# Performance work log

Measured on AMD Instinct MI355X. Metric: run time of the kernel, lower is better.

Reference implementation:

```python
import jax, jax.numpy as jnp
import numpy as np

H = 256  # hidden/feature size (input_size == output_size)
B = 512  # batch
T = 256  # sequence length


def _lstm_cell(x_t, h, c, W_ih, W_hh, b_ih, b_hh):
    # PyTorch gate order: input, forget, cell(g), output
    z = x_t @ W_ih.T + h @ W_hh.T + (b_ih + b_hh)
    i, f, g, o = jnp.split(z, 4, axis=-1)
    c_new = jax.nn.sigmoid(f) * c + jax.nn.sigmoid(i) * jnp.tanh(g)
    h_new = jax.nn.sigmoid(o) * jnp.tanh(c_new)
    return h_new, c_new


def setup_inputs() -> dict:
    key = jax.random.key(0)
    ks = jax.random.split(key, 11)
    s = 1.0 / np.sqrt(H)
    u = lambda k, shape: jax.random.uniform(k, shape, jnp.float32, -s, s)
    return {
        "x": jax.random.normal(ks[0], (B, T, H), jnp.float32),
        "W_ih1": u(ks[1], (4 * H, H)),
        "W_hh1": u(ks[2], (4 * H, H)),
        "b_ih1": u(ks[3], (4 * H,)),
        "b_hh1": u(ks[4], (4 * H,)),
        "W1": u(ks[5], (H, H)),
        "b1": u(ks[6], (H,)),
        "W_ih2": u(ks[7], (4 * H, H)),
        "W_hh2": u(ks[8], (4 * H, H)),
        "b_ih2": u(ks[9], (4 * H,)),
        "b_hh2": u(ks[10], (4 * H,)),
    }


def reference(x, W_ih1, W_hh1, b_ih1, b_hh1, W1, b1, W_ih2, W_hh2, b_ih2, b_hh2):
    Bx, Tx, Hx = x.shape
    xs = jnp.swapaxes(x, 0, 1)  # (T, B, H)

    # Encoder LSTM: only final (h, c) is used downstream
    def enc_step(carry, x_t):
        h, c = carry
        h, c = _lstm_cell(x_t, h, c, W_ih1, W_hh1, b_ih1, b_hh1)
        return (h, c), None

    zeros = jnp.zeros((Bx, Hx), x.dtype)
    (h1, c1), _ = jax.lax.scan(enc_step, (zeros, zeros), xs)

    # x_end = Linear(h1)
    x_end = h1 @ W1.T + b1  # (B, H)

    # Decoder LSTM: feeds its own output back, T steps
    def dec_step(carry, _):
        out, h, c = carry
        h, c = _lstm_cell(out, h, c, W_ih2, W_hh2, b_ih2, b_hh2)
        return (h, h, c), h

    _, outs = jax.lax.scan(dec_step, (x_end, h1, c1), None, length=Tx)  # (T, B, H)

    # Faithful index replay: x_out[:, T-2-i] = outs[i]; i = T-1 hits index -1,
    # overwriting the x_end initially written at position T-1.
    # => x_out[:, j] = outs[T-2-j] for j < T-1, x_out[:, T-1] = outs[T-1]
    x_out_t = jnp.concatenate([outs[: Tx - 1][::-1], outs[Tx - 1 :]], axis=0)  # (T, B, H)
    return jnp.swapaxes(x_out_t, 0, 1)  # (B, T, H)
```

## Files before the change

### kernel.cpp

```cpp
#include <hip/hip_runtime.h>
#include <stdint.h>


#define H_ 256
#define B_ 512
#define T_ 256

typedef short short8 __attribute__((ext_vector_type(8)));
typedef float f32x4 __attribute__((ext_vector_type(4)));

__device__ __forceinline__ short f2bf(float f) {
  union { float f; uint32_t u; } v; v.f = f;
  uint32_t r = (v.u + 0x7FFFu + ((v.u >> 16) & 1u)) >> 16;
  return (short)(uint16_t)r;
}

__device__ __forceinline__ short8 load8f_bf(const float* __restrict__ p) {
  const float4 a = *(const float4*)p;
  const float4 b = *(const float4*)(p + 4);
  short8 r;
  r[0]=f2bf(a.x); r[1]=f2bf(a.y); r[2]=f2bf(a.z); r[3]=f2bf(a.w);
  r[4]=f2bf(b.x); r[5]=f2bf(b.y); r[6]=f2bf(b.z); r[7]=f2bf(b.w);
  return r;
}

__device__ __forceinline__ short8 load8f_bf_sum(const float* __restrict__ p,
                                                const float* __restrict__ q) {
  const float4 a = *(const float4*)p, b = *(const float4*)(p + 4);
  const float4 c = *(const float4*)q, d = *(const float4*)(q + 4);
  short8 r;
  r[0]=f2bf(a.x+c.x); r[1]=f2bf(a.y+c.y); r[2]=f2bf(a.z+c.z); r[3]=f2bf(a.w+c.w);
  r[4]=f2bf(b.x+d.x); r[5]=f2bf(b.y+d.y); r[6]=f2bf(b.z+d.z); r[7]=f2bf(b.w+d.w);
  return r;
}

__device__ __forceinline__ short8 coh_load16(const uint16_t* p) {
  union { uint64_t u[2]; short8 v; } r;
  const uint64_t* q = (const uint64_t*)p;
  r.u[0] = __hip_atomic_load(q,     __ATOMIC_RELAXED, __HIP_MEMORY_SCOPE_AGENT);
  r.u[1] = __hip_atomic_load(q + 1, __ATOMIC_RELAXED, __HIP_MEMORY_SCOPE_AGENT);
  return r.v;
}

__device__ __forceinline__ float sigm(float x)  { return 1.0f / (1.0f + __expf(-x)); }
__device__ __forceinline__ float tanh_(float x) { return 1.0f - 2.0f / (1.0f + __expf(2.0f * x)); }

__global__ __launch_bounds__(256, 1) void encdec_kernel(
    const float* __restrict__ x,
    const float* __restrict__ Wih1, const float* __restrict__ Whh1,
    const float* __restrict__ bih1, const float* __restrict__ bhh1,
    const float* __restrict__ W1,   const float* __restrict__ b1,
    const float* __restrict__ Wih2, const float* __restrict__ Whh2,
    const float* __restrict__ bih2, const float* __restrict__ bhh2,
    float* __restrict__ out,
    uint32_t* __restrict__ bar,
    uint16_t* __restrict__ hbuf)
{
  __shared__ uint16_t hsh[32][16];
  __shared__ float    osh[32][16];

  const int tid = threadIdx.x;
  const int l   = tid & 63;
  const int w   = tid >> 6;
  const int blk = blockIdx.x;
  const int gid = (blk & 7) | ((blk >> 7) << 3);
  const int mid = (blk >> 3) & 15;
  const int bg  = gid * 32;
  const int c0  = mid * 16 + w * 4;

  const int nl   = l & 15;
  const int kc   = l >> 4;
  const int gate = nl >> 2;
  const int cm   = nl & 3;
  const int colg = c0 + cm;
  const int grow = gate * H_ + colg;

  uint32_t* flags = bar + (size_t)gid * 512;
  const int myflag = (mid * 4 + w) * 8;

  uint16_t* slot0 = hbuf;
  uint16_t* slot1 = hbuf + (size_t)B_ * H_;
  uint16_t* slot2 = hbuf + (size_t)2 * B_ * H_;

  auto arrive = [&](int target) {
    asm volatile("s_waitcnt vmcnt(0)" ::: "memory");
    if (l == 0)
      __hip_atomic_store(&flags[myflag], (uint32_t)target,
                         __ATOMIC_RELAXED, __HIP_MEMORY_SCOPE_AGENT);
  };
  auto poll = [&](int target) {
    int g = 0;
    while ((int)__hip_atomic_load(&flags[l * 8], __ATOMIC_RELAXED,
                                  __HIP_MEMORY_SCOPE_AGENT) < target) {
      __builtin_amdgcn_s_sleep(1);
      if (++g > 2000000) break;
    }
    asm volatile("" ::: "memory");
  };
  auto ldsbar = [&]() {
    asm volatile("s_waitcnt lgkmcnt(0)\n\ts_barrier" ::: "memory");
  };

  short8 fwa[8], fwb[8];
#pragma unroll
  for (int kt = 0; kt < 8; ++kt) {
    fwa[kt] = load8f_bf(Wih1 + (size_t)grow * H_ + kt * 32 + kc * 8);
    fwb[kt] = load8f_bf(Whh1 + (size_t)grow * H_ + kt * 32 + kc * 8);
  }
  float bias = bih1[grow] + bhh1[grow];

  float cst[2][4];
#pragma unroll
  for (int mt = 0; mt < 2; ++mt)
#pragma unroll
    for (int r = 0; r < 4; ++r) cst[mt][r] = 0.0f;

  auto epi = [&](const f32x4* acc, float bias_, bool wout) {
    const int rb = (l & 48) | cm;
#pragma unroll
    for (int mt = 0; mt < 2; ++mt) {
      float hn = 0.f;
#pragma unroll
      for (int r = 0; r < 4; ++r) {
        float z = acc[mt][r] + bias_;
        float a = (gate == 2) ? tanh_(z) : sigm(z);
        float ti = __shfl(a, rb,      64);
        float tf = __shfl(a, rb | 4,  64);
        float tg = __shfl(a, rb | 8,  64);
        float to = __shfl(a, rb | 12, 64);
        float cn = tf * cst[mt][r] + ti * tg;
        cst[mt][r] = cn;
        if (r == gate) hn = to * tanh_(cn);
      }
      hsh[mt * 16 + kc * 4 + gate][w * 4 + cm] = (uint16_t)f2bf(hn);
      if (wout) osh[mt * 16 + kc * 4 + gate][w * 4 + cm] = hn;
    }
  };

  const int gb = tid >> 3;
  const int gc = tid & 7;

  f32x4 accN[2];
  auto xmfma = [&](int t) {
#pragma unroll
    for (int mt = 0; mt < 2; ++mt) {
      f32x4 a = {0.f, 0.f, 0.f, 0.f};
      const float* xr = x + ((size_t)(bg + mt * 16 + nl) * T_ + t) * H_ + kc * 8;
#pragma unroll
      for (int kt = 0; kt < 8; ++kt) {
        short8 af = load8f_bf(xr + kt * 32);
        a = __builtin_amdgcn_mfma_f32_16x16x32_bf16(af, fwa[kt], a, 0, 0, 0);
      }
      accN[mt] = a;
    }
  };
  xmfma(0);

  for (int t = 0; t < T_; ++t) {
    f32x4 acc[2] = { accN[0], accN[1] };
    if (t > 0) {
      poll(t);
      const uint16_t* hs = (t & 1) ? slot1 : slot0;
      short8 hA[2][8];
#pragma unroll
      for (int mt = 0; mt < 2; ++mt)
#pragma unroll
        for (int kt = 0; kt < 8; ++kt)
          hA[mt][kt] = coh_load16(hs + (size_t)(bg + mt * 16 + nl) * H_ + kt * 32 + kc * 8);
#pragma unroll
      for (int mt = 0; mt < 2; ++mt)
#pragma unroll
        for (int kt = 0; kt < 8; ++kt)
          acc[mt] = __builtin_amdgcn_mfma_f32_16x16x32_bf16(hA[mt][kt], fwb[kt], acc[mt], 0, 0, 0);
    }
    epi(acc, bias, false);
    ldsbar();
    uint16_t* hw = ((t + 1) & 1) ? slot1 : slot0;
    {
      uint32_t hv = *(const uint32_t*)&hsh[gb][gc * 2];
      __hip_atomic_store((uint32_t*)&hw[(size_t)(bg + gb) * H_ + mid * 16 + gc * 2], hv,
                         __ATOMIC_RELAXED, __HIP_MEMORY_SCOPE_AGENT);
    }
    arrive(t + 1);
    if (t + 1 < T_) xmfma(t + 1);
  }

  poll(T_);
  {
    const int xcol = mid * 16 + nl;
    short8 fw1[8];
#pragma unroll
    for (int kt = 0; kt < 8; ++kt)
      fw1[kt] = load8f_bf(W1 + (size_t)xcol * H_ + kt * 32 + kc * 8);
    f32x4 acc[2] = { {0.f,0.f,0.f,0.f}, {0.f,0.f,0.f,0.f} };
#pragma unroll
    for (int mt = 0; mt < 2; ++mt) {
      const uint16_t* hr = slot0 + (size_t)(bg + mt * 16 + nl) * H_ + kc * 8;
#pragma unroll
      for (int kt = 0; kt < 8; ++kt) {
        short8 af = coh_load16(hr + kt * 32);
        acc[mt] = __builtin_amdgcn_mfma_f32_16x16x32_bf16(af, fw1[kt], acc[mt], 0, 0, 0);
      }
    }
    float bb = b1[xcol];
    if (w == 0) {
#pragma unroll
      for (int mt = 0; mt < 2; ++mt)
#pragma unroll
        for (int r = 0; r < 4; ++r) {
          int b = bg + mt * 16 + kc * 4 + r;
          __hip_atomic_store(&slot2[(size_t)b * H_ + mid * 16 + nl], (uint16_t)f2bf(acc[mt][r] + bb),
                             __ATOMIC_RELAXED, __HIP_MEMORY_SCOPE_AGENT);
        }
    }
  }
  arrive(T_ + 1);

  short8 fwa2[8], fwb2[8], fws[8];
#pragma unroll
  for (int kt = 0; kt < 8; ++kt) {
    const float* pa = Wih2 + (size_t)grow * H_ + kt * 32 + kc * 8;
    const float* pb = Whh2 + (size_t)grow * H_ + kt * 32 + kc * 8;
    fwa2[kt] = load8f_bf(pa);
    fwb2[kt] = load8f_bf(pb);
    fws[kt]  = load8f_bf_sum(pa, pb);
  }
  bias = bih2[grow] + bhh2[grow];
  poll(T_ + 1);

  {
    f32x4 acc[2] = { {0.f,0.f,0.f,0.f}, {0.f,0.f,0.f,0.f} };
    short8 hA[2][8], hB[2][8];
#pragma unroll
    for (int mt = 0; mt < 2; ++mt)
#pragma unroll
      for (int kt = 0; kt < 8; ++kt) {
        const size_t ro = (size_t)(bg + mt * 16 + nl) * H_ + kt * 32 + kc * 8;
        hA[mt][kt] = coh_load16(slot2 + ro);
        hB[mt][kt] = coh_load16(slot0 + ro);
      }
#pragma unroll
    for (int mt = 0; mt < 2; ++mt)
#pragma unroll
      for (int kt = 0; kt < 8; ++kt) {
        acc[mt] = __builtin_amdgcn_mfma_f32_16x16x32_bf16(hA[mt][kt], fwa2[kt], acc[mt], 0, 0, 0);
        acc[mt] = __builtin_amdgcn_mfma_f32_16x16x32_bf16(hB[mt][kt], fwb2[kt], acc[mt], 0, 0, 0);
      }
    epi(acc, bias, true);
    ldsbar();
    uint32_t hv = *(const uint32_t*)&hsh[gb][gc * 2];
    uint64_t ov = *(const uint64_t*)&osh[gb][gc * 2];
    __hip_atomic_store((uint32_t*)&slot1[(size_t)(bg + gb) * H_ + mid * 16 + gc * 2], hv,
                       __ATOMIC_RELAXED, __HIP_MEMORY_SCOPE_AGENT);
    arrive(T_ + 2);
    *(uint64_t*)&out[((size_t)(bg + gb) * T_ + (T_ - 2)) * H_ + mid * 16 + gc * 2] = ov;
  }

  for (int t = 1; t < T_; ++t) {
    poll(T_ + 1 + t);
    const uint16_t* hs = (t & 1) ? slot1 : slot0;
    f32x4 acc[2] = { {0.f,0.f,0.f,0.f}, {0.f,0.f,0.f,0.f} };
    short8 hA[2][8];
#pragma unroll
    for (int mt = 0; mt < 2; ++mt)
#pragma unroll
      for (int kt = 0; kt < 8; ++kt)
        hA[mt][kt] = coh_load16(hs + (size_t)(bg + mt * 16 + nl) * H_ + kt * 32 + kc * 8);
#pragma unroll
    for (int mt = 0; mt < 2; ++mt)
#pragma unroll
      for (int kt = 0; kt < 8; ++kt)
        acc[mt] = __builtin_amdgcn_mfma_f32_16x16x32_bf16(hA[mt][kt], fws[kt], acc[mt], 0, 0, 0);

    epi(acc, bias, true);
    ldsbar();
    const int j = (t == T_ - 1) ? (T_ - 1) : (T_ - 2 - t);
    uint32_t hv = *(const uint32_t*)&hsh[gb][gc * 2];
    uint64_t ov = *(const uint64_t*)&osh[gb][gc * 2];
    if (t + 1 < T_) {
      uint16_t* hw = ((t + 1) & 1) ? slot1 : slot0;
      __hip_atomic_store((uint32_t*)&hw[(size_t)(bg + gb) * H_ + mid * 16 + gc * 2], hv,
                         __ATOMIC_RELAXED, __HIP_MEMORY_SCOPE_AGENT);
      arrive(T_ + 2 + t);
    }
    *(uint64_t*)&out[((size_t)(bg + gb) * T_ + j) * H_ + mid * 16 + gc * 2] = ov;
  }
}

extern "C" void kernel_launch(void* const* d_in, const int* in_sizes, int n_in,
                              void* d_out, int out_size, void* d_ws, size_t ws_size,
                              hipStream_t stream) {
  const float* x    = (const float*)d_in[0];
  const float* Wih1 = (const float*)d_in[1];
  const float* Whh1 = (const float*)d_in[2];
  const float* bih1 = (const float*)d_in[3];
  const float* bhh1 = (const float*)d_in[4];
  const float* W1   = (const float*)d_in[5];
  const float* b1   = (const float*)d_in[6];
  const float* Wih2 = (const float*)d_in[7];
  const float* Whh2 = (const float*)d_in[8];
  const float* bih2 = (const float*)d_in[9];
  const float* bhh2 = (const float*)d_in[10];
  float* out = (float*)d_out;

  uint32_t* bar  = (uint32_t*)d_ws;
  uint16_t* hbuf = (uint16_t*)((char*)d_ws + 32768);

  hipLaunchKernelGGL(encdec_kernel, dim3(256), dim3(256), 0, stream,
                     x, Wih1, Whh1, bih1, bhh1, W1, b1, Wih2, Whh2, bih2, bhh2,
                     out, bar, hbuf);
}
```

Baseline: 4.418 ms.

## Add XCD-local fast coherence path and stage recurrent h through swizzled LDS

At startup, blocks in a batch group check whether they all run on the same XCD and test a handshake. If they pass, the kernel uses sc0-only loads and stores in inline asm for flags and h exchange in place of agent-scope atomics, on the idea that L2 coherence within one XCD is enough. Each step now loads h into a swizzled LDS tile with wide dwordx4 loads, shared across the waves, so each wave no longer issues many small 64-bit atomic loads. The cost is an extra LDS barrier per step, an untested fast path whose correctness depends on how blocks are placed, and a shorter poll timeout.

```diff
diff --git a/kernel.cpp b/kernel.cpp
--- a/kernel.cpp
+++ b/kernel.cpp
@@ -8,6 +8,7 @@
 
 typedef short short8 __attribute__((ext_vector_type(8)));
 typedef float f32x4 __attribute__((ext_vector_type(4)));
+typedef uint32_t u32x4 __attribute__((ext_vector_type(4)));
 
 __device__ __forceinline__ short f2bf(float f) {
   union { float f; uint32_t u; } v; v.f = f;
@@ -34,18 +35,46 @@
   return r;
 }
 
-__device__ __forceinline__ short8 coh_load16(const uint16_t* p) {
-  union { uint64_t u[2]; short8 v; } r;
-  const uint64_t* q = (const uint64_t*)p;
-  r.u[0] = __hip_atomic_load(q,     __ATOMIC_RELAXED, __HIP_MEMORY_SCOPE_AGENT);
-  r.u[1] = __hip_atomic_load(q + 1, __ATOMIC_RELAXED, __HIP_MEMORY_SCOPE_AGENT);
-  return r.v;
+__device__ __forceinline__ void fence4u(u32x4 (&a)[4]) {
+  asm volatile("s_waitcnt vmcnt(0)"
+               : "+v"(a[0]), "+v"(a[1]), "+v"(a[2]), "+v"(a[3]));
+}
+
+template<bool FAST>
+__device__ __forceinline__ uint32_t ldflag(const uint32_t* p) {
+  if constexpr (FAST) {
+    uint32_t r;
+    asm volatile("global_load_dword %0, %1, off sc0\n\ts_waitcnt vmcnt(0)"
+                 : "=v"(r) : "v"((uint64_t)p));
+    return r;
+  } else {
+    return __hip_atomic_load(p, __ATOMIC_RELAXED, __HIP_MEMORY_SCOPE_AGENT);
+  }
+}
+
+template<bool FAST>
+__device__ __forceinline__ void st4(uint32_t* p, uint32_t v) {
+  if constexpr (FAST)
+    asm volatile("global_store_dword %0, %1, off sc0"
+                 :: "v"((uint64_t)p), "v"(v) : "memory");
+  else
+    __hip_atomic_store(p, v, __ATOMIC_RELAXED, __HIP_MEMORY_SCOPE_AGENT);
+}
+
+template<bool FAST>
+__device__ __forceinline__ void st2(uint16_t* p, uint16_t v) {
+  if constexpr (FAST)
+    asm volatile("global_store_short %0, %1, off sc0"
+                 :: "v"((uint64_t)p), "v"((uint32_t)v) : "memory");
+  else
+    __hip_atomic_store(p, v, __ATOMIC_RELAXED, __HIP_MEMORY_SCOPE_AGENT);
 }
 
 __device__ __forceinline__ float sigm(float x)  { return 1.0f / (1.0f + __expf(-x)); }
 __device__ __forceinline__ float tanh_(float x) { return 1.0f - 2.0f / (1.0f + __expf(2.0f * x)); }
 
-__global__ __launch_bounds__(256, 1) void encdec_kernel(
+template<bool FAST>
+__device__ __forceinline__ void body(
     const float* __restrict__ x,
     const float* __restrict__ Wih1, const float* __restrict__ Whh1,
     const float* __restrict__ bih1, const float* __restrict__ bhh1,
@@ -54,11 +83,10 @@
     const float* __restrict__ bih2, const float* __restrict__ bhh2,
     float* __restrict__ out,
     uint32_t* __restrict__ bar,
-    uint16_t* __restrict__ hbuf)
+    uint16_t* __restrict__ hbuf,
+    uint16_t (&hsh)[32][16], float (&osh)[32][16],
+    uint16_t (&hstage)[32][256], uint16_t (&hstage2)[32][256])
 {
-  __shared__ uint16_t hsh[32][16];
-  __shared__ float    osh[32][16];
-
   const int tid = threadIdx.x;
   const int l   = tid & 63;
   const int w   = tid >> 6;
@@ -75,6 +103,8 @@
   const int colg = c0 + cm;
   const int grow = gate * H_ + colg;
 
+  const int POLL_MAX = FAST ? 50000 : 2000000;
+
   uint32_t* flags = bar + (size_t)gid * 512;
   const int myflag = (mid * 4 + w) * 8;
 
@@ -84,21 +114,49 @@
 
   auto arrive = [&](int target) {
     asm volatile("s_waitcnt vmcnt(0)" ::: "memory");
-    if (l == 0)
-      __hip_atomic_store(&flags[myflag], (uint32_t)target,
-                         __ATOMIC_RELAXED, __HIP_MEMORY_SCOPE_AGENT);
+    if (l == 0) st4<FAST>(&flags[myflag], (uint32_t)target);
   };
   auto poll = [&](int target) {
     int g = 0;
-    while ((int)__hip_atomic_load(&flags[l * 8], __ATOMIC_RELAXED,
-                                  __HIP_MEMORY_SCOPE_AGENT) < target) {
+    while ((int)ldflag<FAST>(&flags[l * 8]) < target) {
       __builtin_amdgcn_s_sleep(1);
-      if (++g > 2000000) break;
+      if (++g > POLL_MAX) break;
     }
     asm volatile("" ::: "memory");
   };
   auto ldsbar = [&]() {
     asm volatile("s_waitcnt lgkmcnt(0)\n\ts_barrier" ::: "memory");
+  };
+
+  auto stage_to = [&](uint16_t (&dst)[32][256], const uint16_t* hs) {
+    const int rb_ = tid >> 3;
+    const int cb_ = (tid & 7) * 4;
+    const uint16_t* src = hs + (size_t)(bg + rb_) * H_ + cb_ * 8;
+    if constexpr (FAST) {
+      u32x4 v[4];
+#pragma unroll
+      for (int i = 0; i < 4; ++i)
+        asm volatile("global_load_dwordx4 %0, %1, off sc0"
+                     : "=v"(v[i]) : "v"((uint64_t)(src + i * 8)));
+      fence4u(v);
+#pragma unroll
+      for (int i = 0; i < 4; ++i)
+        *(u32x4*)&dst[rb_][(((cb_ + i) ^ (rb_ & 7)) * 8)] = v[i];
+    } else {
+#pragma unroll
+      for (int i = 0; i < 4; ++i) {
+        union { uint64_t u[2]; u32x4 v; } r;
+        const uint64_t* q = (const uint64_t*)(src + i * 8);
+        r.u[0] = __hip_atomic_load(q,     __ATOMIC_RELAXED, __HIP_MEMORY_SCOPE_AGENT);
+        r.u[1] = __hip_atomic_load(q + 1, __ATOMIC_RELAXED, __HIP_MEMORY_SCOPE_AGENT);
+        *(u32x4*)&dst[rb_][(((cb_ + i) ^ (rb_ & 7)) * 8)] = r.v;
+      }
+    }
+  };
+  auto frag = [&](uint16_t (&src)[32][256], int mt, int kt) -> short8 {
+    const int row = mt * 16 + nl;
+    const int ch  = (kt * 4 + kc) ^ (row & 7);
+    return *(const short8*)&src[row][ch * 8];
   };
 
   short8 fwa[8], fwb[8];
@@ -161,31 +219,28 @@
     if (t > 0) {
       poll(t);
       const uint16_t* hs = (t & 1) ? slot1 : slot0;
-      short8 hA[2][8];
+      stage_to(hstage, hs);
+      ldsbar();
 #pragma unroll
       for (int mt = 0; mt < 2; ++mt)
 #pragma unroll
         for (int kt = 0; kt < 8; ++kt)
-          hA[mt][kt] = coh_load16(hs + (size_t)(bg + mt * 16 + nl) * H_ + kt * 32 + kc * 8);
-#pragma unroll
-      for (int mt = 0; mt < 2; ++mt)
-#pragma unroll
-        for (int kt = 0; kt < 8; ++kt)
-          acc[mt] = __builtin_amdgcn_mfma_f32_16x16x32_bf16(hA[mt][kt], fwb[kt], acc[mt], 0, 0, 0);
+          acc[mt] = __builtin_amdgcn_mfma_f32_16x16x32_bf16(frag(hstage, mt, kt), fwb[kt], acc[mt], 0, 0, 0);
     }
     epi(acc, bias, false);
     ldsbar();
     uint16_t* hw = ((t + 1) & 1) ? slot1 : slot0;
     {
       uint32_t hv = *(const uint32_t*)&hsh[gb][gc * 2];
-      __hip_atomic_store((uint32_t*)&hw[(size_t)(bg + gb) * H_ + mid * 16 + gc * 2], hv,
-                         __ATOMIC_RELAXED, __HIP_MEMORY_SCOPE_AGENT);
+      st4<FAST>((uint32_t*)&hw[(size_t)(bg + gb) * H_ + mid * 16 + gc * 2], hv);
     }
     arrive(t + 1);
     if (t + 1 < T_) xmfma(t + 1);
   }
 
   poll(T_);
+  stage_to(hstage, slot0);
+  ldsbar();
   {
     const int xcol = mid * 16 + nl;
     short8 fw1[8];
@@ -194,14 +249,10 @@
       fw1[kt] = load8f_bf(W1 + (size_t)xcol * H_ + kt * 32 + kc * 8);
     f32x4 acc[2] = { {0.f,0.f,0.f,0.f}, {0.f,0.f,0.f,0.f} };
 #pragma unroll
-    for (int mt = 0; mt < 2; ++mt) {
-      const uint16_t* hr = slot0 + (size_t)(bg + mt * 16 + nl) * H_ + kc * 8;
-#pragma unroll
-      for (int kt = 0; kt < 8; ++kt) {
-        short8 af = coh_load16(hr + kt * 32);
-        acc[mt] = __builtin_amdgcn_mfma_f32_16x16x32_bf16(af, fw1[kt], acc[mt], 0, 0, 0);
-      }
-    }
+    for (int mt = 0; mt < 2; ++mt)
+#pragma unroll
+      for (int kt = 0; kt < 8; ++kt)
+        acc[mt] = __builtin_amdgcn_mfma_f32_16x16x32_bf16(frag(hstage, mt, kt), fw1[kt], acc[mt], 0, 0, 0);
     float bb = b1[xcol];
     if (w == 0) {
 #pragma unroll
@@ -209,8 +260,7 @@
 #pragma unroll
         for (int r = 0; r < 4; ++r) {
           int b = bg + mt * 16 + kc * 4 + r;
-          __hip_atomic_store(&slot2[(size_t)b * H_ + mid * 16 + nl], (uint16_t)f2bf(acc[mt][r] + bb),
-                             __ATOMIC_RELAXED, __HIP_MEMORY_SCOPE_AGENT);
+          st2<FAST>(&slot2[(size_t)b * H_ + mid * 16 + nl], (uint16_t)f2bf(acc[mt][r] + bb));
         }
     }
   }
@@ -229,29 +279,21 @@
   poll(T_ + 1);
 
   {
+    stage_to(hstage2, slot2);
+    ldsbar();
     f32x4 acc[2] = { {0.f,0.f,0.f,0.f}, {0.f,0.f,0.f,0.f} };
-    short8 hA[2][8], hB[2][8];
 #pragma unroll
     for (int mt = 0; mt < 2; ++mt)
 #pragma unroll
       for (int kt = 0; kt < 8; ++kt) {
-        const size_t ro = (size_t)(bg + mt * 16 + nl) * H_ + kt * 32 + kc * 8;
-        hA[mt][kt] = coh_load16(slot2 + ro);
-        hB[mt][kt] = coh_load16(slot0 + ro);
-      }
-#pragma unroll
-    for (int mt = 0; mt < 2; ++mt)
-#pragma unroll
-      for (int kt = 0; kt < 8; ++kt) {
-        acc[mt] = __builtin_amdgcn_mfma_f32_16x16x32_bf16(hA[mt][kt], fwa2[kt], acc[mt], 0, 0, 0);
-        acc[mt] = __builtin_amdgcn_mfma_f32_16x16x32_bf16(hB[mt][kt], fwb2[kt], acc[mt], 0, 0, 0);
+        acc[mt] = __builtin_amdgcn_mfma_f32_16x16x32_bf16(frag(hstage2, mt, kt), fwa2[kt], acc[mt], 0, 0, 0);
+        acc[mt] = __builtin_amdgcn_mfma_f32_16x16x32_bf16(frag(hstage,  mt, kt), fwb2[kt], acc[mt], 0, 0, 0);
       }
     epi(acc, bias, true);
     ldsbar();
     uint32_t hv = *(const uint32_t*)&hsh[gb][gc * 2];
     uint64_t ov = *(const uint64_t*)&osh[gb][gc * 2];
-    __hip_atomic_store((uint32_t*)&slot1[(size_t)(bg + gb) * H_ + mid * 16 + gc * 2], hv,
-                       __ATOMIC_RELAXED, __HIP_MEMORY_SCOPE_AGENT);
+    st4<FAST>((uint32_t*)&slot1[(size_t)(bg + gb) * H_ + mid * 16 + gc * 2], hv);
     arrive(T_ + 2);
     *(uint64_t*)&out[((size_t)(bg + gb) * T_ + (T_ - 2)) * H_ + mid * 16 + gc * 2] = ov;
   }
@@ -259,18 +301,14 @@
   for (int t = 1; t < T_; ++t) {
     poll(T_ + 1 + t);
     const uint16_t* hs = (t & 1) ? slot1 : slot0;
+    stage_to(hstage, hs);
+    ldsbar();
     f32x4 acc[2] = { {0.f,0.f,0.f,0.f}, {0.f,0.f,0.f,0.f} };
-    short8 hA[2][8];
 #pragma unroll
     for (int mt = 0; mt < 2; ++mt)
 #pragma unroll
       for (int kt = 0; kt < 8; ++kt)
-        hA[mt][kt] = coh_load16(hs + (size_t)(bg + mt * 16 + nl) * H_ + kt * 32 + kc * 8);
-#pragma unroll
-    for (int mt = 0; mt < 2; ++mt)
-#pragma unroll
-      for (int kt = 0; kt < 8; ++kt)
-        acc[mt] = __builtin_amdgcn_mfma_f32_16x16x32_bf16(hA[mt][kt], fws[kt], acc[mt], 0, 0, 0);
+        acc[mt] = __builtin_amdgcn_mfma_f32_16x16x32_bf16(frag(hstage, mt, kt), fws[kt], acc[mt], 0, 0, 0);
 
     epi(acc, bias, true);
     ldsbar();
@@ -279,12 +317,83 @@
     uint64_t ov = *(const uint64_t*)&osh[gb][gc * 2];
     if (t + 1 < T_) {
       uint16_t* hw = ((t + 1) & 1) ? slot1 : slot0;
-      __hip_atomic_store((uint32_t*)&hw[(size_t)(bg + gb) * H_ + mid * 16 + gc * 2], hv,
-                         __ATOMIC_RELAXED, __HIP_MEMORY_SCOPE_AGENT);
+      st4<FAST>((uint32_t*)&hw[(size_t)(bg + gb) * H_ + mid * 16 + gc * 2], hv);
       arrive(T_ + 2 + t);
     }
     *(uint64_t*)&out[((size_t)(bg + gb) * T_ + j) * H_ + mid * 16 + gc * 2] = ov;
   }
+}
+
+__global__ __launch_bounds__(256, 1) void encdec_kernel(
+    const float* __restrict__ x,
+    const float* __restrict__ Wih1, const float* __restrict__ Whh1,
+    const float* __restrict__ bih1, const float* __restrict__ bhh1,
+    const float* __restrict__ W1,   const float* __restrict__ b1,
+    const float* __restrict__ Wih2, const float* __restrict__ Whh2,
+    const float* __restrict__ bih2, const float* __restrict__ bhh2,
+    float* __restrict__ out,
+    uint32_t* __restrict__ bar,
+    uint16_t* __restrict__ hbuf)
+{
+  __shared__ __align__(16) uint16_t hstage [32][256];
+  __shared__ __align__(16) uint16_t hstage2[32][256];
+  __shared__ uint16_t hsh[32][16];
+  __shared__ float    osh[32][16];
+
+  const int tid = threadIdx.x;
+  const int l   = tid & 63;
+  const int blk = blockIdx.x;
+  const int gid = (blk & 7) | ((blk >> 7) << 3);
+  const int mid = (blk >> 3) & 15;
+
+  uint32_t* xw = bar + (size_t)gid * 512;
+
+  const uint32_t my_xcc = (uint32_t)__builtin_amdgcn_s_getreg(6164) & 0xffu;
+  if (tid == 0)
+    __hip_atomic_store(&xw[mid * 8 + 1], 0x100u | my_xcc,
+                       __ATOMIC_RELAXED, __HIP_MEMORY_SCOPE_AGENT);
+  uint32_t pv = 0; int g = 0; bool seen = true;
+  for (;;) {
+    pv = __hip_atomic_load(&xw[(l & 15) * 8 + 1],
+                           __ATOMIC_RELAXED, __HIP_MEMORY_SCOPE_AGENT);
+    if (pv & 0x100u) break;
+    __builtin_amdgcn_s_sleep(1);
+    if (++g > 1000000) { seen = false; break; }
+  }
+  const bool same_xcd = __all((int)(seen && ((pv & 0xffu) == my_xcc)));
+
+  int verdict = 0;
+  if (same_xcd) {
+    if (tid == 0) st4<true>(&xw[mid * 8 + 2], 0xA5A5u);
+    g = 0; bool s2 = true;
+    for (;;) {
+      uint32_t qv = ldflag<true>(&xw[(l & 15) * 8 + 2]);
+      if (qv == 0xA5A5u) break;
+      __builtin_amdgcn_s_sleep(1);
+      if (++g > 20000) { s2 = false; break; }
+    }
+    verdict = __all((int)s2) ? 1 : 0;
+  }
+
+  if (tid == 0)
+    __hip_atomic_store(&xw[mid * 8 + 3], 0x200u | (uint32_t)verdict,
+                       __ATOMIC_RELAXED, __HIP_MEMORY_SCOPE_AGENT);
+  uint32_t vv = 0; g = 0; seen = true;
+  for (;;) {
+    vv = __hip_atomic_load(&xw[(l & 15) * 8 + 3],
+                           __ATOMIC_RELAXED, __HIP_MEMORY_SCOPE_AGENT);
+    if (vv & 0x200u) break;
+    __builtin_amdgcn_s_sleep(1);
+    if (++g > 1000000) { seen = false; break; }
+  }
+  const bool fast = __all((int)(seen && (vv & 1u)));
+
+  if (fast)
+    body<true>(x, Wih1, Whh1, bih1, bhh1, W1, b1, Wih2, Whh2, bih2, bhh2,
+               out, bar, hbuf, hsh, osh, hstage, hstage2);
+  else
+    body<false>(x, Wih1, Whh1, bih1, bhh1, W1, b1, Wih2, Whh2, bih2, bhh2,
+                out, bar, hbuf, hsh, osh, hstage, hstage2);
 }
 
 extern "C" void kernel_launch(void* const* d_in, const int* in_sizes, int n_in,
```

Measured after the change: 6.398 ms. +44.8%, slower.

## Replace flag barrier with tagged-data polling on hidden-state exchange buffers

Applied to the files above, without the earlier changes.

Removes the separate arrive/poll flag handshake between blocks and instead packs a step tag into the upper 32 bits of each 64-bit store of hidden-state data. Consumers spin-load the whole hidden tile and retry until every tag matches the expected step, so data and readiness arrive in one memory round trip instead of a flag wait followed by a data load. The cost is that the exchange buffers double in size, each retry reloads the full tile, and the s_waitcnt before the flag write is gone. The x_end handoff also reuses slot1 with a tag, and the decoder's first step reuses the h1 tile already held in registers.

```diff
diff --git a/kernel.cpp b/kernel.cpp
--- a/kernel.cpp
+++ b/kernel.cpp
@@ -34,14 +34,6 @@
   return r;
 }
 
-__device__ __forceinline__ short8 coh_load16(const uint16_t* p) {
-  union { uint64_t u[2]; short8 v; } r;
-  const uint64_t* q = (const uint64_t*)p;
-  r.u[0] = __hip_atomic_load(q,     __ATOMIC_RELAXED, __HIP_MEMORY_SCOPE_AGENT);
-  r.u[1] = __hip_atomic_load(q + 1, __ATOMIC_RELAXED, __HIP_MEMORY_SCOPE_AGENT);
-  return r.v;
-}
-
 __device__ __forceinline__ float sigm(float x)  { return 1.0f / (1.0f + __expf(-x)); }
 __device__ __forceinline__ float tanh_(float x) { return 1.0f - 2.0f / (1.0f + __expf(2.0f * x)); }
 
@@ -53,8 +45,7 @@
     const float* __restrict__ Wih2, const float* __restrict__ Whh2,
     const float* __restrict__ bih2, const float* __restrict__ bhh2,
     float* __restrict__ out,
-    uint32_t* __restrict__ bar,
-    uint16_t* __restrict__ hbuf)
+    uint64_t* __restrict__ s0, uint64_t* __restrict__ s1)
 {
   __shared__ uint16_t hsh[32][16];
   __shared__ float    osh[32][16];
@@ -66,36 +57,59 @@
   const int gid = (blk & 7) | ((blk >> 7) << 3);
   const int mid = (blk >> 3) & 15;
   const int bg  = gid * 32;
-  const int c0  = mid * 16 + w * 4;
 
   const int nl   = l & 15;
   const int kc   = l >> 4;
   const int gate = nl >> 2;
   const int cm   = nl & 3;
-  const int colg = c0 + cm;
+  const int colg = mid * 16 + w * 4 + cm;
   const int grow = gate * H_ + colg;
 
-  uint32_t* flags = bar + (size_t)gid * 512;
-  const int myflag = (mid * 4 + w) * 8;
-
-  uint16_t* slot0 = hbuf;
-  uint16_t* slot1 = hbuf + (size_t)B_ * H_;
-  uint16_t* slot2 = hbuf + (size_t)2 * B_ * H_;
-
-  auto arrive = [&](int target) {
-    asm volatile("s_waitcnt vmcnt(0)" ::: "memory");
-    if (l == 0)
-      __hip_atomic_store(&flags[myflag], (uint32_t)target,
-                         __ATOMIC_RELAXED, __HIP_MEMORY_SCOPE_AGENT);
-  };
-  auto poll = [&](int target) {
-    int g = 0;
-    while ((int)__hip_atomic_load(&flags[l * 8], __ATOMIC_RELAXED,
-                                  __HIP_MEMORY_SCOPE_AGENT) < target) {
-      __builtin_amdgcn_s_sleep(1);
-      if (++g > 2000000) break;
-    }
-    asm volatile("" ::: "memory");
+  uint64_t* slot[2] = { s0, s1 };
+  int budget = 1 << 20;
+
+  auto ld_tile = [&](const uint64_t* s, uint32_t tag, short8 (&hA)[2][8]) {
+    uint64_t raw[2][8][4];
+    for (;;) {
+#pragma unroll
+      for (int mt = 0; mt < 2; ++mt) {
+        const uint64_t* rp = s + (size_t)(bg + mt * 16 + nl) * (H_ / 2) + kc * 4;
+#pragma unroll
+        for (int kt = 0; kt < 8; ++kt)
+#pragma unroll
+          for (int i = 0; i < 4; ++i)
+            raw[mt][kt][i] = __hip_atomic_load(rp + kt * 16 + i,
+                                               __ATOMIC_RELAXED, __HIP_MEMORY_SCOPE_AGENT);
+      }
+      uint32_t bad = 0;
+#pragma unroll
+      for (int mt = 0; mt < 2; ++mt)
+#pragma unroll
+        for (int kt = 0; kt < 8; ++kt)
+#pragma unroll
+          for (int i = 0; i < 4; ++i)
+            bad |= ((uint32_t)(raw[mt][kt][i] >> 32)) ^ tag;
+      if (__all(bad == 0) || --budget < 0) break;
+    }
+#pragma unroll
+    for (int mt = 0; mt < 2; ++mt)
+#pragma unroll
+      for (int kt = 0; kt < 8; ++kt) {
+        union { uint32_t d[4]; short8 v; } u;
+#pragma unroll
+        for (int i = 0; i < 4; ++i) u.d[i] = (uint32_t)raw[mt][kt][i];
+        hA[mt][kt] = u.v;
+      }
+  };
+
+  const int gb = tid >> 3;
+  const int gc = tid & 7;
+
+  auto stg = [&](uint64_t* s, uint32_t tag) {
+    uint32_t pay = (uint32_t)hsh[gb][gc * 2] | ((uint32_t)hsh[gb][gc * 2 + 1] << 16);
+    __hip_atomic_store(s + (size_t)(bg + gb) * (H_ / 2) + mid * 8 + gc,
+                       ((uint64_t)tag << 32) | pay,
+                       __ATOMIC_RELAXED, __HIP_MEMORY_SCOPE_AGENT);
   };
   auto ldsbar = [&]() {
     asm volatile("s_waitcnt lgkmcnt(0)\n\ts_barrier" ::: "memory");
@@ -137,9 +151,6 @@
     }
   };
 
-  const int gb = tid >> 3;
-  const int gc = tid & 7;
-
   f32x4 accN[2];
   auto xmfma = [&](int t) {
 #pragma unroll
@@ -159,14 +170,8 @@
   for (int t = 0; t < T_; ++t) {
     f32x4 acc[2] = { accN[0], accN[1] };
     if (t > 0) {
-      poll(t);
-      const uint16_t* hs = (t & 1) ? slot1 : slot0;
       short8 hA[2][8];
-#pragma unroll
-      for (int mt = 0; mt < 2; ++mt)
-#pragma unroll
-        for (int kt = 0; kt < 8; ++kt)
-          hA[mt][kt] = coh_load16(hs + (size_t)(bg + mt * 16 + nl) * H_ + kt * 32 + kc * 8);
+      ld_tile(slot[t & 1], (uint32_t)t, hA);
 #pragma unroll
       for (int mt = 0; mt < 2; ++mt)
 #pragma unroll
@@ -175,17 +180,12 @@
     }
     epi(acc, bias, false);
     ldsbar();
-    uint16_t* hw = ((t + 1) & 1) ? slot1 : slot0;
-    {
-      uint32_t hv = *(const uint32_t*)&hsh[gb][gc * 2];
-      __hip_atomic_store((uint32_t*)&hw[(size_t)(bg + gb) * H_ + mid * 16 + gc * 2], hv,
-                         __ATOMIC_RELAXED, __HIP_MEMORY_SCOPE_AGENT);
-    }
-    arrive(t + 1);
+    stg(slot[(t + 1) & 1], (uint32_t)(t + 1));
     if (t + 1 < T_) xmfma(t + 1);
   }
 
-  poll(T_);
+  short8 h1f[2][8];
+  ld_tile(slot[0], 256u, h1f);
   {
     const int xcol = mid * 16 + nl;
     short8 fw1[8];
@@ -194,27 +194,29 @@
       fw1[kt] = load8f_bf(W1 + (size_t)xcol * H_ + kt * 32 + kc * 8);
     f32x4 acc[2] = { {0.f,0.f,0.f,0.f}, {0.f,0.f,0.f,0.f} };
 #pragma unroll
-    for (int mt = 0; mt < 2; ++mt) {
-      const uint16_t* hr = slot0 + (size_t)(bg + mt * 16 + nl) * H_ + kc * 8;
-#pragma unroll
-      for (int kt = 0; kt < 8; ++kt) {
-        short8 af = coh_load16(hr + kt * 32);
-        acc[mt] = __builtin_amdgcn_mfma_f32_16x16x32_bf16(af, fw1[kt], acc[mt], 0, 0, 0);
-      }
-    }
+    for (int mt = 0; mt < 2; ++mt)
+#pragma unroll
+      for (int kt = 0; kt < 8; ++kt)
+        acc[mt] = __builtin_amdgcn_mfma_f32_16x16x32_bf16(h1f[mt][kt], fw1[kt], acc[mt], 0, 0, 0);
     float bb = b1[xcol];
     if (w == 0) {
 #pragma unroll
       for (int mt = 0; mt < 2; ++mt)
 #pragma unroll
         for (int r = 0; r < 4; ++r) {
-          int b = bg + mt * 16 + kc * 4 + r;
-          __hip_atomic_store(&slot2[(size_t)b * H_ + mid * 16 + nl], (uint16_t)f2bf(acc[mt][r] + bb),
-                             __ATOMIC_RELAXED, __HIP_MEMORY_SCOPE_AGENT);
+          float me = acc[mt][r] + bb;
+          float nb = __shfl(me, l ^ 1, 64);
+          if (!(nl & 1)) {
+            uint32_t pay = (uint32_t)(uint16_t)f2bf(me) |
+                           ((uint32_t)(uint16_t)f2bf(nb) << 16);
+            __hip_atomic_store(slot[1] + (size_t)(bg + mt * 16 + kc * 4 + r) * (H_ / 2)
+                                       + mid * 8 + (nl >> 1),
+                               ((uint64_t)257u << 32) | pay,
+                               __ATOMIC_RELAXED, __HIP_MEMORY_SCOPE_AGENT);
+          }
         }
     }
   }
-  arrive(T_ + 1);
 
   short8 fwa2[8], fwb2[8], fws[8];
 #pragma unroll
@@ -226,63 +228,39 @@
     fws[kt]  = load8f_bf_sum(pa, pb);
   }
   bias = bih2[grow] + bhh2[grow];
-  poll(T_ + 1);
 
   {
+    short8 xeF[2][8];
+    ld_tile(slot[1], 257u, xeF);
     f32x4 acc[2] = { {0.f,0.f,0.f,0.f}, {0.f,0.f,0.f,0.f} };
-    short8 hA[2][8], hB[2][8];
 #pragma unroll
     for (int mt = 0; mt < 2; ++mt)
 #pragma unroll
       for (int kt = 0; kt < 8; ++kt) {
-        const size_t ro = (size_t)(bg + mt * 16 + nl) * H_ + kt * 32 + kc * 8;
-        hA[mt][kt] = coh_load16(slot2 + ro);
-        hB[mt][kt] = coh_load16(slot0 + ro);
-      }
-#pragma unroll
-    for (int mt = 0; mt < 2; ++mt)
-#pragma unroll
-      for (int kt = 0; kt < 8; ++kt) {
-        acc[mt] = __builtin_amdgcn_mfma_f32_16x16x32_bf16(hA[mt][kt], fwa2[kt], acc[mt], 0, 0, 0);
-        acc[mt] = __builtin_amdgcn_mfma_f32_16x16x32_bf16(hB[mt][kt], fwb2[kt], acc[mt], 0, 0, 0);
+        acc[mt] = __builtin_amdgcn_mfma_f32_16x16x32_bf16(xeF[mt][kt], fwa2[kt], acc[mt], 0, 0, 0);
+        acc[mt] = __builtin_amdgcn_mfma_f32_16x16x32_bf16(h1f[mt][kt], fwb2[kt], acc[mt], 0, 0, 0);
       }
     epi(acc, bias, true);
     ldsbar();
-    uint32_t hv = *(const uint32_t*)&hsh[gb][gc * 2];
     uint64_t ov = *(const uint64_t*)&osh[gb][gc * 2];
-    __hip_atomic_store((uint32_t*)&slot1[(size_t)(bg + gb) * H_ + mid * 16 + gc * 2], hv,
-                       __ATOMIC_RELAXED, __HIP_MEMORY_SCOPE_AGENT);
-    arrive(T_ + 2);
+    stg(slot[0], 258u);
     *(uint64_t*)&out[((size_t)(bg + gb) * T_ + (T_ - 2)) * H_ + mid * 16 + gc * 2] = ov;
   }
 
   for (int t = 1; t < T_; ++t) {
-    poll(T_ + 1 + t);
-    const uint16_t* hs = (t & 1) ? slot1 : slot0;
+    short8 hA[2][8];
+    ld_tile(slot[(257 + t) & 1], (uint32_t)(257 + t), hA);
     f32x4 acc[2] = { {0.f,0.f,0.f,0.f}, {0.f,0.f,0.f,0.f} };
-    short8 hA[2][8];
-#pragma unroll
-    for (int mt = 0; mt < 2; ++mt)
-#pragma unroll
-      for (int kt = 0; kt < 8; ++kt)
-        hA[mt][kt] = coh_load16(hs + (size_t)(bg + mt * 16 + nl) * H_ + kt * 32 + kc * 8);
 #pragma unroll
     for (int mt = 0; mt < 2; ++mt)
 #pragma unroll
       for (int kt = 0; kt < 8; ++kt)
         acc[mt] = __builtin_amdgcn_mfma_f32_16x16x32_bf16(hA[mt][kt], fws[kt], acc[mt], 0, 0, 0);
-
     epi(acc, bias, true);
     ldsbar();
     const int j = (t == T_ - 1) ? (T_ - 1) : (T_ - 2 - t);
-    uint32_t hv = *(const uint32_t*)&hsh[gb][gc * 2];
     uint64_t ov = *(const uint64_t*)&osh[gb][gc * 2];
-    if (t + 1 < T_) {
-      uint16_t* hw = ((t + 1) & 1) ? slot1 : slot0;
-      __hip_atomic_store((uint32_t*)&hw[(size_t)(bg + gb) * H_ + mid * 16 + gc * 2], hv,
-                         __ATOMIC_RELAXED, __HIP_MEMORY_SCOPE_AGENT);
-      arrive(T_ + 2 + t);
-    }
+    if (t + 1 < T_) stg(slot[(258 + t) & 1], (uint32_t)(258 + t));
     *(uint64_t*)&out[((size_t)(bg + gb) * T_ + j) * H_ + mid * 16 + gc * 2] = ov;
   }
 }
@@ -303,10 +281,10 @@
   const float* bhh2 = (const float*)d_in[10];
   float* out = (float*)d_out;
 
-  uint32_t* bar  = (uint32_t*)d_ws;
-  uint16_t* hbuf = (uint16_t*)((char*)d_ws + 32768);
+  uint64_t* s0 = (uint64_t*)d_ws;
+  uint64_t* s1 = s0 + (size_t)B_ * (H_ / 2);
 
   hipLaunchKernelGGL(encdec_kernel, dim3(256), dim3(256), 0, stream,
                      x, Wih1, Whh1, bih1, bhh1, W1, b1, Wih2, Whh2, bih2, bhh2,
-                     out, bar, hbuf);
-}
+                     out, s0, s1);
+}
```

Result: slower. 7.500 ms (+69.8%).

## Shrink grid to 64 blocks with four column tiles per wave

Applied to the files above, without the earlier changes.

Each block now owns 64 hidden columns (four 16x16 MFMA n-tiles per wave) instead of 16, so the grid drops from 256 to 64 blocks. Each batch group's per-step barrier now waits on 16 flags instead of 64. Each loaded h fragment is reused across four weight tiles, which cuts global h traffic and the h-publish store count. The cost is more serial MFMA and epilogue work per wave, far fewer active CUs, and much higher register pressure from the weight fragments, which risks spills.

```diff
diff --git a/kernel.cpp b/kernel.cpp
--- a/kernel.cpp
+++ b/kernel.cpp
@@ -56,24 +56,22 @@
     uint32_t* __restrict__ bar,
     uint16_t* __restrict__ hbuf)
 {
-  __shared__ uint16_t hsh[32][16];
-  __shared__ float    osh[32][16];
+  __shared__ __align__(16) uint16_t hsh[32][64];
+  __shared__ __align__(16) float    osh[32][64];
 
   const int tid = threadIdx.x;
   const int l   = tid & 63;
   const int w   = tid >> 6;
   const int blk = blockIdx.x;
-  const int gid = (blk & 7) | ((blk >> 7) << 3);
-  const int mid = (blk >> 3) & 15;
+  const int gid = (blk & 7) | ((blk >> 5) << 3);
+  const int mid = (blk >> 3) & 3;
   const int bg  = gid * 32;
-  const int c0  = mid * 16 + w * 4;
+  const int cbase = mid * 64 + w * 16;
 
   const int nl   = l & 15;
   const int kc   = l >> 4;
   const int gate = nl >> 2;
   const int cm   = nl & 3;
-  const int colg = c0 + cm;
-  const int grow = gate * H_ + colg;
 
   uint32_t* flags = bar + (size_t)gid * 512;
   const int myflag = (mid * 4 + w) * 8;
@@ -90,7 +88,7 @@
   };
   auto poll = [&](int target) {
     int g = 0;
-    while ((int)__hip_atomic_load(&flags[l * 8], __ATOMIC_RELAXED,
+    while ((int)__hip_atomic_load(&flags[(l & 15) * 8], __ATOMIC_RELAXED,
                                   __HIP_MEMORY_SCOPE_AGENT) < target) {
       __builtin_amdgcn_s_sleep(1);
       if (++g > 2000000) break;
@@ -101,93 +99,121 @@
     asm volatile("s_waitcnt lgkmcnt(0)\n\ts_barrier" ::: "memory");
   };
 
-  short8 fwa[8], fwb[8];
-#pragma unroll
-  for (int kt = 0; kt < 8; ++kt) {
-    fwa[kt] = load8f_bf(Wih1 + (size_t)grow * H_ + kt * 32 + kc * 8);
-    fwb[kt] = load8f_bf(Whh1 + (size_t)grow * H_ + kt * 32 + kc * 8);
-  }
-  float bias = bih1[grow] + bhh1[grow];
-
-  float cst[2][4];
+  auto grow = [&](int nt) { return gate * H_ + cbase + nt * 4 + cm; };
+
+  short8 fwa[4][8], fwb[4][8];
+  float bias1v[4];
+#pragma unroll
+  for (int nt = 0; nt < 4; ++nt) {
+    const size_t ro = (size_t)grow(nt) * H_;
+#pragma unroll
+    for (int kt = 0; kt < 8; ++kt) {
+      fwa[nt][kt] = load8f_bf(Wih1 + ro + kt * 32 + kc * 8);
+      fwb[nt][kt] = load8f_bf(Whh1 + ro + kt * 32 + kc * 8);
+    }
+    bias1v[nt] = bih1[grow(nt)] + bhh1[grow(nt)];
+  }
+
+  float cst[2][4][4];
 #pragma unroll
   for (int mt = 0; mt < 2; ++mt)
 #pragma unroll
-    for (int r = 0; r < 4; ++r) cst[mt][r] = 0.0f;
-
-  auto epi = [&](const f32x4* acc, float bias_, bool wout) {
+    for (int nt = 0; nt < 4; ++nt)
+#pragma unroll
+      for (int r = 0; r < 4; ++r) cst[mt][nt][r] = 0.0f;
+
+  auto epi = [&](const f32x4 (&acc)[2][4], const float* biasv, bool wout) {
     const int rb = (l & 48) | cm;
 #pragma unroll
-    for (int mt = 0; mt < 2; ++mt) {
-      float hn = 0.f;
-#pragma unroll
-      for (int r = 0; r < 4; ++r) {
-        float z = acc[mt][r] + bias_;
-        float a = (gate == 2) ? tanh_(z) : sigm(z);
-        float ti = __shfl(a, rb,      64);
-        float tf = __shfl(a, rb | 4,  64);
-        float tg = __shfl(a, rb | 8,  64);
-        float to = __shfl(a, rb | 12, 64);
-        float cn = tf * cst[mt][r] + ti * tg;
-        cst[mt][r] = cn;
-        if (r == gate) hn = to * tanh_(cn);
-      }
-      hsh[mt * 16 + kc * 4 + gate][w * 4 + cm] = (uint16_t)f2bf(hn);
-      if (wout) osh[mt * 16 + kc * 4 + gate][w * 4 + cm] = hn;
-    }
+    for (int mt = 0; mt < 2; ++mt)
+#pragma unroll
+      for (int nt = 0; nt < 4; ++nt) {
+        float hn = 0.f;
+#pragma unroll
+        for (int r = 0; r < 4; ++r) {
+          float z = acc[mt][nt][r] + biasv[nt];
+          float a = (gate == 2) ? tanh_(z) : sigm(z);
+          float ti = __shfl(a, rb,      64);
+          float tf = __shfl(a, rb | 4,  64);
+          float tg = __shfl(a, rb | 8,  64);
+          float to = __shfl(a, rb | 12, 64);
+          float cn = tf * cst[mt][nt][r] + ti * tg;
+          cst[mt][nt][r] = cn;
+          if (r == gate) hn = to * tanh_(cn);
+        }
+        hsh[mt * 16 + kc * 4 + gate][w * 16 + nt * 4 + cm] = (uint16_t)f2bf(hn);
+        if (wout) osh[mt * 16 + kc * 4 + gate][w * 16 + nt * 4 + cm] = hn;
+      }
   };
 
   const int gb = tid >> 3;
   const int gc = tid & 7;
 
-  f32x4 accN[2];
+  auto pub_h = [&](uint16_t* hw) {
+    uint64_t v0 = *(const uint64_t*)&hsh[gb][gc * 8];
+    uint64_t v1 = *(const uint64_t*)&hsh[gb][gc * 8 + 4];
+    uint64_t* d = (uint64_t*)&hw[(size_t)(bg + gb) * H_ + mid * 64 + gc * 8];
+    __hip_atomic_store(d,     v0, __ATOMIC_RELAXED, __HIP_MEMORY_SCOPE_AGENT);
+    __hip_atomic_store(d + 1, v1, __ATOMIC_RELAXED, __HIP_MEMORY_SCOPE_AGENT);
+  };
+  auto pub_out = [&](int j) {
+    float* d = &out[((size_t)(bg + gb) * T_ + j) * H_ + mid * 64 + gc * 8];
+    const float* s = &osh[gb][gc * 8];
+    *(uint64_t*)(d + 0) = *(const uint64_t*)(s + 0);
+    *(uint64_t*)(d + 2) = *(const uint64_t*)(s + 2);
+    *(uint64_t*)(d + 4) = *(const uint64_t*)(s + 4);
+    *(uint64_t*)(d + 6) = *(const uint64_t*)(s + 6);
+  };
+
+  f32x4 accN[2][4];
   auto xmfma = [&](int t) {
 #pragma unroll
     for (int mt = 0; mt < 2; ++mt) {
-      f32x4 a = {0.f, 0.f, 0.f, 0.f};
       const float* xr = x + ((size_t)(bg + mt * 16 + nl) * T_ + t) * H_ + kc * 8;
+#pragma unroll
+      for (int nt = 0; nt < 4; ++nt) accN[mt][nt] = (f32x4){0.f, 0.f, 0.f, 0.f};
 #pragma unroll
       for (int kt = 0; kt < 8; ++kt) {
         short8 af = load8f_bf(xr + kt * 32);
-        a = __builtin_amdgcn_mfma_f32_16x16x32_bf16(af, fwa[kt], a, 0, 0, 0);
-      }
-      accN[mt] = a;
+#pragma unroll
+        for (int nt = 0; nt < 4; ++nt)
+          accN[mt][nt] = __builtin_amdgcn_mfma_f32_16x16x32_bf16(af, fwa[nt][kt], accN[mt][nt], 0, 0, 0);
+      }
     }
   };
   xmfma(0);
 
   for (int t = 0; t < T_; ++t) {
-    f32x4 acc[2] = { accN[0], accN[1] };
+    f32x4 acc[2][4];
+#pragma unroll
+    for (int mt = 0; mt < 2; ++mt)
+#pragma unroll
+      for (int nt = 0; nt < 4; ++nt) acc[mt][nt] = accN[mt][nt];
     if (t > 0) {
       poll(t);
       const uint16_t* hs = (t & 1) ? slot1 : slot0;
-      short8 hA[2][8];
-#pragma unroll
-      for (int mt = 0; mt < 2; ++mt)
-#pragma unroll
-        for (int kt = 0; kt < 8; ++kt)
-          hA[mt][kt] = coh_load16(hs + (size_t)(bg + mt * 16 + nl) * H_ + kt * 32 + kc * 8);
-#pragma unroll
-      for (int mt = 0; mt < 2; ++mt)
-#pragma unroll
-        for (int kt = 0; kt < 8; ++kt)
-          acc[mt] = __builtin_amdgcn_mfma_f32_16x16x32_bf16(hA[mt][kt], fwb[kt], acc[mt], 0, 0, 0);
-    }
-    epi(acc, bias, false);
+#pragma unroll
+      for (int mt = 0; mt < 2; ++mt) {
+        const uint16_t* hr = hs + (size_t)(bg + mt * 16 + nl) * H_ + kc * 8;
+#pragma unroll
+        for (int kt = 0; kt < 8; ++kt) {
+          short8 hA = coh_load16(hr + kt * 32);
+#pragma unroll
+          for (int nt = 0; nt < 4; ++nt)
+            acc[mt][nt] = __builtin_amdgcn_mfma_f32_16x16x32_bf16(hA, fwb[nt][kt], acc[mt][nt], 0, 0, 0);
+        }
+      }
+    }
+    epi(acc, bias1v, false);
     ldsbar();
-    uint16_t* hw = ((t + 1) & 1) ? slot1 : slot0;
-    {
-      uint32_t hv = *(const uint32_t*)&hsh[gb][gc * 2];
-      __hip_atomic_store((uint32_t*)&hw[(size_t)(bg + gb) * H_ + mid * 16 + gc * 2], hv,
-                         __ATOMIC_RELAXED, __HIP_MEMORY_SCOPE_AGENT);
-    }
+    pub_h(((t + 1) & 1) ? slot1 : slot0);
     arrive(t + 1);
     if (t + 1 < T_) xmfma(t + 1);
   }
 
   poll(T_);
   {
-    const int xcol = mid * 16 + nl;
+    const int xcol = cbase + nl;
     short8 fw1[8];
 #pragma unroll
     for (int kt = 0; kt < 8; ++kt)
@@ -203,87 +229,96 @@
       }
     }
     float bb = b1[xcol];
-    if (w == 0) {
-#pragma unroll
-      for (int mt = 0; mt < 2; ++mt)
-#pragma unroll
-        for (int r = 0; r < 4; ++r) {
-          int b = bg + mt * 16 + kc * 4 + r;
-          __hip_atomic_store(&slot2[(size_t)b * H_ + mid * 16 + nl], (uint16_t)f2bf(acc[mt][r] + bb),
-                             __ATOMIC_RELAXED, __HIP_MEMORY_SCOPE_AGENT);
+#pragma unroll
+    for (int mt = 0; mt < 2; ++mt)
+#pragma unroll
+      for (int r = 0; r < 4; ++r) {
+        int b = bg + mt * 16 + kc * 4 + r;
+        __hip_atomic_store(&slot2[(size_t)b * H_ + xcol], (uint16_t)f2bf(acc[mt][r] + bb),
+                           __ATOMIC_RELAXED, __HIP_MEMORY_SCOPE_AGENT);
+      }
+  }
+  arrive(T_ + 1);
+
+  short8 fwa2[4][8], fwb2[4][8];
+  float bias2v[4];
+#pragma unroll
+  for (int nt = 0; nt < 4; ++nt) {
+    const size_t ro = (size_t)(gate * H_ + cbase + nt * 4 + cm) * H_;
+#pragma unroll
+    for (int kt = 0; kt < 8; ++kt) {
+      fwa2[nt][kt] = load8f_bf(Wih2 + ro + kt * 32 + kc * 8);
+      fwb2[nt][kt] = load8f_bf(Whh2 + ro + kt * 32 + kc * 8);
+    }
+    const int g2 = gate * H_ + cbase + nt * 4 + cm;
+    bias2v[nt] = bih2[g2] + bhh2[g2];
+  }
+  poll(T_ + 1);
+
+  {
+    f32x4 acc[2][4];
+#pragma unroll
+    for (int mt = 0; mt < 2; ++mt)
+#pragma unroll
+      for (int nt = 0; nt < 4; ++nt) acc[mt][nt] = (f32x4){0.f, 0.f, 0.f, 0.f};
+#pragma unroll
+    for (int mt = 0; mt < 2; ++mt) {
+      const size_t ro = (size_t)(bg + mt * 16 + nl) * H_ + kc * 8;
+#pragma unroll
+      for (int kt = 0; kt < 8; ++kt) {
+        short8 hA = coh_load16(slot2 + ro + kt * 32);
+        short8 hB = coh_load16(slot0 + ro + kt * 32);
+#pragma unroll
+        for (int nt = 0; nt < 4; ++nt) {
+          acc[mt][nt] = __builtin_amdgcn_mfma_f32_16x16x32_bf16(hA, fwa2[nt][kt], acc[mt][nt], 0, 0, 0);
+          acc[mt][nt] = __builtin_amdgcn_mfma_f32_16x16x32_bf16(hB, fwb2[nt][kt], acc[mt][nt], 0, 0, 0);
         }
-    }
-  }
-  arrive(T_ + 1);
-
-  short8 fwa2[8], fwb2[8], fws[8];
-#pragma unroll
-  for (int kt = 0; kt < 8; ++kt) {
-    const float* pa = Wih2 + (size_t)grow * H_ + kt * 32 + kc * 8;
-    const float* pb = Whh2 + (size_t)grow * H_ + kt * 32 + kc * 8;
-    fwa2[kt] = load8f_bf(pa);
-    fwb2[kt] = load8f_bf(pb);
-    fws[kt]  = load8f_bf_sum(pa, pb);
-  }
-  bias = bih2[grow] + bhh2[grow];
-  poll(T_ + 1);
-
-  {
-    f32x4 acc[2] = { {0.f,0.f,0.f,0.f}, {0.f,0.f,0.f,0.f} };
-    short8 hA[2][8], hB[2][8];
-#pragma unroll
-    for (int mt = 0; mt < 2; ++mt)
-#pragma unroll
-      for (int kt = 0; kt < 8; ++kt) {
-        const size_t ro = (size_t)(bg + mt * 16 + nl) * H_ + kt * 32 + kc * 8;
-        hA[mt][kt] = coh_load16(slot2 + ro);
-        hB[mt][kt] = coh_load16(slot0 + ro);
-      }
-#pragma unroll
-    for (int mt = 0; mt < 2; ++mt)
-#pragma unroll
-      for (int kt = 0; kt < 8; ++kt) {
-        acc[mt] = __builtin_amdgcn_mfma_f32_16x16x32_bf16(hA[mt][kt], fwa2[kt], acc[mt], 0, 0, 0);
-        acc[mt] = __builtin_amdgcn_mfma_f32_16x16x32_bf16(hB[mt][kt], fwb2[kt], acc[mt], 0, 0, 0);
-      }
-    epi(acc, bias, true);
+      }
+    }
+    epi(acc, bias2v, true);
     ldsbar();
-    uint32_t hv = *(const uint32_t*)&hsh[gb][gc * 2];
-    uint64_t ov = *(const uint64_t*)&osh[gb][gc * 2];
-    __hip_atomic_store((uint32_t*)&slot1[(size_t)(bg + gb) * H_ + mid * 16 + gc * 2], hv,
-                       __ATOMIC_RELAXED, __HIP_MEMORY_SCOPE_AGENT);
+    pub_h(slot1);
     arrive(T_ + 2);
-    *(uint64_t*)&out[((size_t)(bg + gb) * T_ + (T_ - 2)) * H_ + mid * 16 + gc * 2] = ov;
+    pub_out(T_ - 2);
+  }
+
+  short8 fws[4][8];
+#pragma unroll
+  for (int nt = 0; nt < 4; ++nt) {
+    const size_t ro = (size_t)(gate * H_ + cbase + nt * 4 + cm) * H_;
+#pragma unroll
+    for (int kt = 0; kt < 8; ++kt)
+      fws[nt][kt] = load8f_bf_sum(Wih2 + ro + kt * 32 + kc * 8,
+                                  Whh2 + ro + kt * 32 + kc * 8);
   }
 
   for (int t = 1; t < T_; ++t) {
     poll(T_ + 1 + t);
     const uint16_t* hs = (t & 1) ? slot1 : slot0;
-    f32x4 acc[2] = { {0.f,0.f,0.f,0.f}, {0.f,0.f,0.f,0.f} };
-    short8 hA[2][8];
-#pragma unroll
-    for (int mt = 0; mt < 2; ++mt)
-#pragma unroll
-      for (int kt = 0; kt < 8; ++kt)
-        hA[mt][kt] = coh_load16(hs + (size_t)(bg + mt * 16 + nl) * H_ + kt * 32 + kc * 8);
-#pragma unroll
-    for (int mt = 0; mt < 2; ++mt)
-#pragma unroll
-      for (int kt = 0; kt < 8; ++kt)
-        acc[mt] = __builtin_amdgcn_mfma_f32_16x16x32_bf16(hA[mt][kt], fws[kt], acc[mt], 0, 0, 0);
-
-    epi(acc, bias, true);
+    f32x4 acc[2][4];
+#pragma unroll
+    for (int mt = 0; mt < 2; ++mt)
+#pragma unroll
+      for (int nt = 0; nt < 4; ++nt) acc[mt][nt] = (f32x4){0.f, 0.f, 0.f, 0.f};
+#pragma unroll
+    for (int mt = 0; mt < 2; ++mt) {
+      const uint16_t* hr = hs + (size_t)(bg + mt * 16 + nl) * H_ + kc * 8;
+#pragma unroll
+      for (int kt = 0; kt < 8; ++kt) {
+        short8 hA = coh_load16(hr + kt * 32);
+#pragma unroll
+        for (int nt = 0; nt < 4; ++nt)
+          acc[mt][nt] = __builtin_amdgcn_mfma_f32_16x16x32_bf16(hA, fws[nt][kt], acc[mt][nt], 0, 0, 0);
+      }
+    }
+    epi(acc, bias2v, true);
     ldsbar();
     const int j = (t == T_ - 1) ? (T_ - 1) : (T_ - 2 - t);
-    uint32_t hv = *(const uint32_t*)&hsh[gb][gc * 2];
-    uint64_t ov = *(const uint64_t*)&osh[gb][gc * 2];
     if (t + 1 < T_) {
-      uint16_t* hw = ((t + 1) & 1) ? slot1 : slot0;
-      __hip_atomic_store((uint32_t*)&hw[(size_t)(bg + gb) * H_ + mid * 16 + gc * 2], hv,
-                         __ATOMIC_RELAXED, __HIP_MEMORY_SCOPE_AGENT);
+      pub_h(((t + 1) & 1) ? slot1 : slot0);
       arrive(T_ + 2 + t);
     }
-    *(uint64_t*)&out[((size_t)(bg + gb) * T_ + j) * H_ + mid * 16 + gc * 2] = ov;
+    pub_out(j);
   }
 }
 
@@ -306,7 +341,7 @@
   uint32_t* bar  = (uint32_t*)d_ws;
   uint16_t* hbuf = (uint16_t*)((char*)d_ws + 32768);
 
-  hipLaunchKernelGGL(encdec_kernel, dim3(256), dim3(256), 0, stream,
+  hipLaunchKernelGGL(encdec_kernel, dim3(64), dim3(256), 0, stream,
                      x, Wih1, Whh1, bih1, bhh1, W1, b1, Wih2, Whh2, bih2, bhh2,
                      out, bar, hbuf);
 }
```

After: 7.948 ms. +79.9%, slower.
